# Kernel tuning notes

Hardware: AMD Instinct MI355X
Metric: run time of the kernel (lower is better)

Reference implementation:

```python
import jax, jax.numpy as jnp
import numpy as np

HEADS = 8
DIM_HEAD = 64
MAX_REL = 200  # max_rel_dist


def setup_inputs() -> dict:
    key = jax.random.key(0)
    ks = jax.random.split(key, 5)
    B, N, D = 4, 2048, 512
    x = jax.random.normal(ks[0], (B, N, D), dtype=jnp.float32)
    temporal_mask = jax.random.randint(ks[1], (N, N), 0, 2, dtype=jnp.int32)
    gamma = jnp.ones((D,), jnp.float32)
    beta = jnp.zeros((D,), jnp.float32)
    Wqkv = jax.random.normal(ks[2], (D, 3 * HEADS * DIM_HEAD), dtype=jnp.float32) * 0.02
    Wout = jax.random.normal(ks[3], (HEADS * DIM_HEAD, D), dtype=jnp.float32) * 0.02
    bout = jnp.zeros((D,), jnp.float32)
    rel_table = jax.random.normal(ks[4], (2 * MAX_REL - 1,), dtype=jnp.float32) * 0.02
    return {"x": x, "gamma": gamma, "beta": beta, "Wqkv": Wqkv, "Wout": Wout,
            "bout": bout, "rel_table": rel_table, "temporal_mask": temporal_mask}


def reference(x, gamma, beta, Wqkv, Wout, bout, rel_table, temporal_mask):
    B, N, D = x.shape
    scale = DIM_HEAD ** -0.5
    # LayerNorm
    mu = jnp.mean(x, axis=-1, keepdims=True)
    var = jnp.mean(jnp.square(x - mu), axis=-1, keepdims=True)
    xn = (x - mu) * jax.lax.rsqrt(var + 1e-5) * gamma + beta
    # QKV projection (no bias), split heads: b n (h d) -> b h n d
    qkv = xn @ Wqkv  # [B, N, 3*H*d]
    q, k, v = jnp.split(qkv, 3, axis=-1)
    split = lambda t: t.reshape(B, N, HEADS, DIM_HEAD).transpose(0, 2, 1, 3)
    q, k, v = split(q), split(k), split(v)
    # scores with learned relative-position bias
    dots = jnp.einsum('bhnd,bhmd->bhnm', q, k) * scale  # [B,H,N,N]
    idx = jnp.arange(N)
    rel = jnp.clip(idx[:, None] - idx[None, :], -(MAX_REL - 1), MAX_REL - 1) + MAX_REL - 1
    dots = dots + rel_table[rel][None, None, :, :]
    # temporal mask (0 -> -inf); large negative for grad safety
    dots = jnp.where(temporal_mask[None, None, :, :] == 0, jnp.float32(-1e9), dots)
    attn = jax.nn.softmax(dots, axis=-1)
    out = jnp.einsum('bhnm,bhmd->bhnd', attn, v)
    out = out.transpose(0, 2, 1, 3).reshape(B, N, HEADS * DIM_HEAD)
    return out @ Wout + bout
```

## Files before the change

### kernel.cpp

```cpp
#include <hip/hip_runtime.h>

typedef __attribute__((ext_vector_type(8))) short bf16x8;
typedef __attribute__((ext_vector_type(4))) short bf16x4;
typedef __attribute__((ext_vector_type(4))) float f32x4;
typedef unsigned short ushort_t;

#define B_ 4
#define H_ 8
#define N_ 2048
#define D_ 512
#define MAXREL 199

__device__ __forceinline__ ushort_t f2bf(float f) {
    union { float f; unsigned u; } v; v.f = f;
    unsigned r = v.u + 0x7fffu + ((v.u >> 16) & 1u);
    return (ushort_t)(r >> 16);
}
__device__ __forceinline__ ushort_t f2bf_fast(float f) {
    union { float f; unsigned u; } v; v.f = f;
    return (ushort_t)((v.u + 0x8000u) >> 16);
}
__device__ __forceinline__ float bf2f(ushort_t u) {
    union { unsigned u; float f; } v; v.u = ((unsigned)u) << 16;
    return v.f;
}
__device__ __forceinline__ void gl_lds16(const ushort_t* g, ushort_t* l) {
    __builtin_amdgcn_global_load_lds(
        (const __attribute__((address_space(1))) void*)g,
        (__attribute__((address_space(3))) void*)l,
        16, 0, 0);
}

__global__ __launch_bounds__(256) void ln_kernel(const float* __restrict__ x,
                                                 const float* __restrict__ gamma,
                                                 const float* __restrict__ beta,
                                                 ushort_t* __restrict__ xn) {
    __shared__ float sbuf[4];
    const int row = blockIdx.x;
    const int t = threadIdx.x;
    const float* xr = x + (size_t)row * D_;

    float v0 = xr[t];
    float v1 = xr[t + 256];

    float s = v0 + v1;
    for (int o = 32; o > 0; o >>= 1) s += __shfl_down(s, o);
    if ((t & 63) == 0) sbuf[t >> 6] = s;
    __syncthreads();
    float mu = (sbuf[0] + sbuf[1] + sbuf[2] + sbuf[3]) * (1.0f / D_);
    __syncthreads();

    float d0 = v0 - mu, d1 = v1 - mu;
    float s2 = d0 * d0 + d1 * d1;
    for (int o = 32; o > 0; o >>= 1) s2 += __shfl_down(s2, o);
    if ((t & 63) == 0) sbuf[t >> 6] = s2;
    __syncthreads();
    float var = (sbuf[0] + sbuf[1] + sbuf[2] + sbuf[3]) * (1.0f / D_);
    float rs = rsqrtf(var + 1e-5f);

    ushort_t* yr = xn + (size_t)row * D_;
    yr[t]       = f2bf(d0 * rs * gamma[t]       + beta[t]);
    yr[t + 256] = f2bf(d1 * rs * gamma[t + 256] + beta[t + 256]);
}

__global__ __launch_bounds__(256) void wtrans_kernel(const float* __restrict__ W,
                                                     ushort_t* __restrict__ Wt,
                                                     int K, int Nn) {
    __shared__ float tile[32][33];
    const int bx = blockIdx.x * 32;
    const int by = blockIdx.y * 32;
    const int tx = threadIdx.x & 31, ty = threadIdx.x >> 5;
    #pragma unroll
    for (int i = 0; i < 32; i += 8)
        tile[ty + i][tx] = W[(size_t)(by + ty + i) * Nn + bx + tx];
    __syncthreads();
    #pragma unroll
    for (int i = 0; i < 32; i += 8)
        Wt[(size_t)(bx + ty + i) * K + by + tx] = f2bf(tile[tx][ty + i]);
}

__global__ __launch_bounds__(256) void bias_pack_kernel(const float* __restrict__ rel,
                                                        const int* __restrict__ mask,
                                                        ushort_t* __restrict__ bp) {
    int idx = blockIdx.x * 256 + threadIdx.x;
    int n = idx >> 11, m = idx & 2047;
    int dl = n - m;
    dl = dl < -MAXREL ? -MAXREL : (dl > MAXREL ? MAXREL : dl);
    float v = (mask[idx] == 0) ? -1e9f : rel[dl + MAXREL];
    int jt = m >> 6, m16 = m & 15, nt = (m >> 4) & 3;
    bp[((size_t)n * 32 + jt) * 64 + m16 * 4 + nt] = f2bf(v);
}

__global__ __launch_bounds__(256) void gemm_qkv(const ushort_t* __restrict__ A,
                                                const ushort_t* __restrict__ Bt,
                                                ushort_t* __restrict__ qb,
                                                ushort_t* __restrict__ kb,
                                                ushort_t* __restrict__ vb) {
    __shared__ ushort_t As[128 * 32];
    __shared__ ushort_t Bs[128 * 32];
    const int t = threadIdx.x;
    const int lane = t & 63, w = t >> 6;
    const int m16 = lane & 15, quad = lane >> 4;
    const int wr = w >> 1, wc = w & 1;
    const int r0 = blockIdx.y * 128, c0 = blockIdx.x * 128;

    const ushort_t* Ag = A  + (size_t)(r0 + (t >> 2)) * D_ + (t & 3) * 8;
    const ushort_t* Bg = Bt + (size_t)(c0 + (t >> 2)) * D_ + (t & 3) * 8;
    ushort_t* AsW = As + w * 512;
    ushort_t* BsW = Bs + w * 512;

    f32x4 acc[4][4];
    #pragma unroll
    for (int i = 0; i < 4; i++)
        #pragma unroll
        for (int j = 0; j < 4; j++) acc[i][j] = (f32x4){0.f, 0.f, 0.f, 0.f};

    for (int k0 = 0; k0 < D_; k0 += 32) {
        gl_lds16(Ag + k0, AsW);
        gl_lds16(Ag + k0 + (size_t)64 * D_, AsW + 2048);
        gl_lds16(Bg + k0, BsW);
        gl_lds16(Bg + k0 + (size_t)64 * D_, BsW + 2048);
        __syncthreads();
        bf16x8 af[4], bfr[4];
        #pragma unroll
        for (int rt = 0; rt < 4; rt++)
            af[rt] = *(const bf16x8*)(As + (wr * 64 + rt * 16 + m16) * 32 + quad * 8);
        #pragma unroll
        for (int ct = 0; ct < 4; ct++)
            bfr[ct] = *(const bf16x8*)(Bs + (wc * 64 + ct * 16 + m16) * 32 + quad * 8);
        #pragma unroll
        for (int rt = 0; rt < 4; rt++)
            #pragma unroll
            for (int ct = 0; ct < 4; ct++)
                acc[rt][ct] = __builtin_amdgcn_mfma_f32_16x16x32_bf16(af[rt], bfr[ct], acc[rt][ct], 0, 0, 0);
        __syncthreads();
    }

    #pragma unroll
    for (int ct = 0; ct < 4; ct++) {
        int cc = c0 + wc * 64 + ct * 16;
        int which = cc >> 9;
        int h = (cc >> 6) & 7;
        int d = (cc & 63) + m16;
        #pragma unroll
        for (int rt = 0; rt < 4; rt++) {
            int rowb = r0 + wr * 64 + rt * 16 + quad * 4;
            int b = rowb >> 11, n0 = rowb & 2047;
            if (which == 0) {
                #pragma unroll
                for (int r = 0; r < 4; r++)
                    qb[((size_t)((b * H_ + h) * N_ + n0 + r)) * 64 + d] = f2bf(acc[rt][ct][r] * 0.125f);
            } else if (which == 1) {
                #pragma unroll
                for (int r = 0; r < 4; r++)
                    kb[((size_t)((b * H_ + h) * N_ + n0 + r)) * 64 + d] = f2bf(acc[rt][ct][r]);
            } else {
                union { ushort_t u4[4]; unsigned long long ll; } pk;
                #pragma unroll
                for (int r = 0; r < 4; r++) pk.u4[r] = f2bf(acc[rt][ct][r]);
                *(unsigned long long*)(vb + ((size_t)((b * H_ + h) * 64 + d)) * N_ + n0) = pk.ll;
            }
        }
    }
}

__global__ __launch_bounds__(256) void gemm_out(const ushort_t* __restrict__ A,
                                                const ushort_t* __restrict__ Bt,
                                                const float* __restrict__ bias,
                                                float* __restrict__ C) {
    __shared__ ushort_t As[64 * 32];
    __shared__ ushort_t Bs[128 * 32];
    const int t = threadIdx.x;
    const int lane = t & 63, w = t >> 6;
    const int m16 = lane & 15, quad = lane >> 4;
    const int wr = w >> 1, wc = w & 1;
    const int r0 = blockIdx.y * 64, c0 = blockIdx.x * 128;

    const ushort_t* Ag = A  + (size_t)(r0 + (t >> 2)) * D_ + (t & 3) * 8;
    const ushort_t* Bg = Bt + (size_t)(c0 + (t >> 2)) * D_ + (t & 3) * 8;
    ushort_t* AsW = As + w * 512;
    ushort_t* BsW = Bs + w * 512;

    f32x4 acc[2][4];
    #pragma unroll
    for (int i = 0; i < 2; i++)
        #pragma unroll
        for (int j = 0; j < 4; j++) acc[i][j] = (f32x4){0.f, 0.f, 0.f, 0.f};

    for (int k0 = 0; k0 < D_; k0 += 32) {
        gl_lds16(Ag + k0, AsW);
        gl_lds16(Bg + k0, BsW);
        gl_lds16(Bg + k0 + (size_t)64 * D_, BsW + 2048);
        __syncthreads();
        bf16x8 af[2], bfr[4];
        #pragma unroll
        for (int mf = 0; mf < 2; mf++)
            af[mf] = *(const bf16x8*)(As + (wr * 32 + mf * 16 + m16) * 32 + quad * 8);
        #pragma unroll
        for (int nt = 0; nt < 4; nt++)
            bfr[nt] = *(const bf16x8*)(Bs + (wc * 64 + nt * 16 + m16) * 32 + quad * 8);
        #pragma unroll
        for (int mf = 0; mf < 2; mf++)
            #pragma unroll
            for (int nt = 0; nt < 4; nt++)
                acc[mf][nt] = __builtin_amdgcn_mfma_f32_16x16x32_bf16(af[mf], bfr[nt], acc[mf][nt], 0, 0, 0);
        __syncthreads();
    }

    #pragma unroll
    for (int mf = 0; mf < 2; mf++) {
        #pragma unroll
        for (int nt = 0; nt < 4; nt++) {
            int col = c0 + wc * 64 + nt * 16 + m16;
            int row0 = r0 + wr * 32 + mf * 16 + quad * 4;
            float bv = bias[col];
            #pragma unroll
            for (int r = 0; r < 4; r++)
                C[(size_t)(row0 + r) * 512 + col] = acc[mf][nt][r] + bv;
        }
    }
}

__global__ __launch_bounds__(256, 3) void attn_mfma(const ushort_t* __restrict__ qb,
                                                    const ushort_t* __restrict__ kb,
                                                    const ushort_t* __restrict__ vb,
                                                    const ushort_t* __restrict__ bp,
                                                    ushort_t* __restrict__ attn) {
    __shared__ ushort_t Ks[2][64 * 64];
    __shared__ ushort_t Vs[2][64 * 64];
    __shared__ ushort_t p_s[4 * 2][16 * 64];

    const int t = threadIdx.x;
    const int w = t >> 6, lane = t & 63;
    const int m16 = lane & 15, quad = lane >> 4;
    const int id = blockIdx.x;
    const int bh = id & 31;
    const int qt = id >> 5;
    const int b = bh >> 3, h = bh & 7;
    const int n0w = qt * 128 + w * 32;

    const int srow0 = t >> 3, scb = t & 7;
    const int srow1 = srow0 + 32;
    const int soff0 = srow0 * 64 + (scb ^ (srow0 & 7)) * 8;
    const int soff1 = srow1 * 64 + (scb ^ (srow1 & 7)) * 8;
    const ushort_t* kgbase = kb + ((size_t)bh * N_) * 64;
    const ushort_t* vgbase = vb + ((size_t)bh * 64) * N_;

    const ushort_t* qpb = qb + ((size_t)(bh * N_ + n0w + m16)) * 64 + quad * 8;
    bf16x8 qa[2][2];
    qa[0][0] = *(const bf16x8*)(qpb);
    qa[0][1] = *(const bf16x8*)(qpb + 32);
    qa[1][0] = *(const bf16x8*)(qpb + 16 * 64);
    qa[1][1] = *(const bf16x8*)(qpb + 16 * 64 + 32);

    {
        bf16x8 k0 = *(const bf16x8*)(kgbase + (size_t)srow0 * 64 + scb * 8);
        bf16x8 k1 = *(const bf16x8*)(kgbase + (size_t)srow1 * 64 + scb * 8);
        bf16x8 v0 = *(const bf16x8*)(vgbase + (size_t)srow0 * N_ + scb * 8);
        bf16x8 v1 = *(const bf16x8*)(vgbase + (size_t)srow1 * N_ + scb * 8);
        *(bf16x8*)(&Ks[0][soff0]) = k0;
        *(bf16x8*)(&Ks[0][soff1]) = k1;
        *(bf16x8*)(&Vs[0][soff0]) = v0;
        *(bf16x8*)(&Vs[0][soff1]) = v1;
    }
    __syncthreads();

    f32x4 o[2][4];
    #pragma unroll
    for (int mf = 0; mf < 2; mf++)
        #pragma unroll
        for (int nt = 0; nt < 4; nt++) o[mf][nt] = (f32x4){0.f, 0.f, 0.f, 0.f};
    float rsum[2][4] = {};

    for (int jt = 0; jt < 32; jt++) {
        const int buf = jt & 1;
        const int j0 = jt * 64;
        const bool more = (jt < 31);

        bf16x8 kst0, kst1, vst0, vst1;
        if (more) {
            const ushort_t* kg = kgbase + (size_t)(j0 + 64) * 64;
            const ushort_t* vg = vgbase + (j0 + 64);
            kst0 = *(const bf16x8*)(kg + (size_t)srow0 * 64 + scb * 8);
            kst1 = *(const bf16x8*)(kg + (size_t)srow1 * 64 + scb * 8);
            vst0 = *(const bf16x8*)(vg + (size_t)srow0 * N_ + scb * 8);
            vst1 = *(const bf16x8*)(vg + (size_t)srow1 * N_ + scb * 8);
        }

        bf16x4 bcur[2][4];
        #pragma unroll
        for (int mf = 0; mf < 2; mf++)
            #pragma unroll
            for (int r = 0; r < 4; r++) {
                int n = n0w + mf * 16 + quad * 4 + r;
                bcur[mf][r] = *(const bf16x4*)(bp + ((size_t)n * 32 + jt) * 64 + m16 * 4);
            }

        f32x4 s[2][4];
        #pragma unroll
        for (int nt = 0; nt < 4; nt++) {
            int kr = nt * 16 + m16;
            bf16x8 kf0 = *(const bf16x8*)(&Ks[buf][kr * 64 + ((quad) ^ (kr & 7)) * 8]);
            bf16x8 kf1 = *(const bf16x8*)(&Ks[buf][kr * 64 + ((quad + 4) ^ (kr & 7)) * 8]);
            #pragma unroll
            for (int mf = 0; mf < 2; mf++) {
                f32x4 a2 = (f32x4){0.f, 0.f, 0.f, 0.f};
                a2 = __builtin_amdgcn_mfma_f32_16x16x32_bf16(qa[mf][0], kf0, a2, 0, 0, 0);
                a2 = __builtin_amdgcn_mfma_f32_16x16x32_bf16(qa[mf][1], kf1, a2, 0, 0, 0);
                s[mf][nt] = a2;
            }
        }

        #pragma unroll
        for (int mf = 0; mf < 2; mf++) {
            ushort_t* pw = p_s[w * 2 + mf];
            #pragma unroll
            for (int nt = 0; nt < 4; nt++) {
                int chunk = nt * 2 + (m16 >> 3), pos = m16 & 7;
                #pragma unroll
                for (int r = 0; r < 4; r++) {
                    float p = __expf(s[mf][nt][r] + bf2f((ushort_t)bcur[mf][r][nt]));
                    rsum[mf][r] += p;
                    int row = quad * 4 + r;
                    pw[row * 64 + ((chunk ^ (row & 7)) << 3) + pos] = f2bf_fast(p);
                }
            }
        }

        bf16x8 pa[2][2];
        #pragma unroll
        for (int mf = 0; mf < 2; mf++) {
            const ushort_t* pw = p_s[w * 2 + mf];
            pa[mf][0] = *(const bf16x8*)(pw + m16 * 64 + ((quad ^ (m16 & 7)) << 3));
            pa[mf][1] = *(const bf16x8*)(pw + m16 * 64 + (((quad + 4) ^ (m16 & 7)) << 3));
        }

        #pragma unroll
        for (int nt = 0; nt < 4; nt++) {
            int d = nt * 16 + m16;
            bf16x8 vf0 = *(const bf16x8*)(&Vs[buf][d * 64 + ((quad) ^ (d & 7)) * 8]);
            bf16x8 vf1 = *(const bf16x8*)(&Vs[buf][d * 64 + ((quad + 4) ^ (d & 7)) * 8]);
            #pragma unroll
            for (int mf = 0; mf < 2; mf++) {
                o[mf][nt] = __builtin_amdgcn_mfma_f32_16x16x32_bf16(pa[mf][0], vf0, o[mf][nt], 0, 0, 0);
                o[mf][nt] = __builtin_amdgcn_mfma_f32_16x16x32_bf16(pa[mf][1], vf1, o[mf][nt], 0, 0, 0);
            }
        }

        if (more) {
            *(bf16x8*)(&Ks[buf ^ 1][soff0]) = kst0;
            *(bf16x8*)(&Ks[buf ^ 1][soff1]) = kst1;
            *(bf16x8*)(&Vs[buf ^ 1][soff0]) = vst0;
            *(bf16x8*)(&Vs[buf ^ 1][soff1]) = vst1;
        }
        __syncthreads();
    }

    #pragma unroll
    for (int mf = 0; mf < 2; mf++)
        #pragma unroll
        for (int r = 0; r < 4; r++) {
            float t2 = rsum[mf][r];
            t2 += __shfl_xor(t2, 1);
            t2 += __shfl_xor(t2, 2);
            t2 += __shfl_xor(t2, 4);
            t2 += __shfl_xor(t2, 8);
            float inv = 1.0f / t2;
            int n = n0w + mf * 16 + quad * 4 + r;
            ushort_t* orow = attn + ((size_t)(b * N_ + n)) * 512 + h * 64 + m16;
            #pragma unroll
            for (int nt = 0; nt < 4; nt++) orow[nt * 16] = f2bf(o[mf][nt][r] * inv);
        }
}

extern "C" void kernel_launch(void* const* d_in, const int* in_sizes, int n_in,
                              void* d_out, int out_size, void* d_ws, size_t ws_size,
                              hipStream_t stream) {
    const float* x     = (const float*)d_in[0];
    const float* gamma = (const float*)d_in[1];
    const float* beta  = (const float*)d_in[2];
    const float* Wqkv  = (const float*)d_in[3];
    const float* Wout  = (const float*)d_in[4];
    const float* bout  = (const float*)d_in[5];
    const float* rel   = (const float*)d_in[6];
    const int*   mask  = (const int*)d_in[7];
    float* out = (float*)d_out;

    char* wsb = (char*)d_ws;
    ushort_t* xn    = (ushort_t*)(wsb);
    ushort_t* attnb = (ushort_t*)(wsb + ( 8u << 20));
    ushort_t* qb    = (ushort_t*)(wsb + (16u << 20));
    ushort_t* kb    = (ushort_t*)(wsb + (24u << 20));
    ushort_t* vb    = (ushort_t*)(wsb + (32u << 20));
    ushort_t* WqkvT = (ushort_t*)(wsb + (40u << 20));
    ushort_t* WoutT = (ushort_t*)(wsb + (42u << 20));
    ushort_t* bp    = (ushort_t*)(wsb + (44u << 20));

    wtrans_kernel<<<dim3(1536 / 32, 512 / 32), 256, 0, stream>>>(Wqkv, WqkvT, 512, 1536);
    wtrans_kernel<<<dim3(512 / 32, 512 / 32), 256, 0, stream>>>(Wout, WoutT, 512, 512);
    bias_pack_kernel<<<(N_ * N_) / 256, 256, 0, stream>>>(rel, mask, bp);

    ln_kernel<<<B_ * N_, 256, 0, stream>>>(x, gamma, beta, xn);

    gemm_qkv<<<dim3(1536 / 128, 8192 / 128), 256, 0, stream>>>(xn, WqkvT, qb, kb, vb);

    attn_mfma<<<512, 256, 0, stream>>>(qb, kb, vb, bp, attnb);

    gemm_out<<<dim3(512 / 128, 8192 / 64), 256, 0, stream>>>(attnb, WoutT, bout, out);
}
```

Before: 214.1 us.

## Merge prep kernels into one launch and use 8-wave attention blocks

Folds the weight transposes, bias packing and LayerNorm into a single prep kernel that dispatches on block index, which saves three launches. The attention kernel moves to 512 threads per block, each wave owning 16 query rows instead of 32, so each K/V tile staged in LDS is shared by twice as many waves and each thread loads half as much. The trade is that every wave now reads the K/V fragments from LDS for half as much MFMA work, which raises the LDS traffic per FLOP. The launch bound also changes to (512, 4), which may cap registers.

New measurement: 200.4 us. -6.4%, faster.

```diff
diff --git a/kernel.cpp b/kernel.cpp
--- a/kernel.cpp
+++ b/kernel.cpp
@@ -31,64 +31,73 @@
         16, 0, 0);
 }
 
-__global__ __launch_bounds__(256) void ln_kernel(const float* __restrict__ x,
-                                                 const float* __restrict__ gamma,
-                                                 const float* __restrict__ beta,
-                                                 ushort_t* __restrict__ xn) {
-    __shared__ float sbuf[4];
-    const int row = blockIdx.x;
+#define PREP_BIAS  16384
+#define PREP_LN    8192
+#define PREP_WQ    768
+#define PREP_WO    256
+__global__ __launch_bounds__(256) void prep_kernel(const float* __restrict__ x,
+                                                   const float* __restrict__ gamma,
+                                                   const float* __restrict__ beta,
+                                                   ushort_t* __restrict__ xn,
+                                                   const float* __restrict__ Wqkv,
+                                                   ushort_t* __restrict__ WqkvT,
+                                                   const float* __restrict__ Wout,
+                                                   ushort_t* __restrict__ WoutT,
+                                                   const float* __restrict__ rel,
+                                                   const int* __restrict__ mask,
+                                                   ushort_t* __restrict__ bp) {
+    __shared__ float smem[32 * 33];
+    const int blk = blockIdx.x;
     const int t = threadIdx.x;
-    const float* xr = x + (size_t)row * D_;
-
-    float v0 = xr[t];
-    float v1 = xr[t + 256];
-
-    float s = v0 + v1;
-    for (int o = 32; o > 0; o >>= 1) s += __shfl_down(s, o);
-    if ((t & 63) == 0) sbuf[t >> 6] = s;
-    __syncthreads();
-    float mu = (sbuf[0] + sbuf[1] + sbuf[2] + sbuf[3]) * (1.0f / D_);
-    __syncthreads();
-
-    float d0 = v0 - mu, d1 = v1 - mu;
-    float s2 = d0 * d0 + d1 * d1;
-    for (int o = 32; o > 0; o >>= 1) s2 += __shfl_down(s2, o);
-    if ((t & 63) == 0) sbuf[t >> 6] = s2;
-    __syncthreads();
-    float var = (sbuf[0] + sbuf[1] + sbuf[2] + sbuf[3]) * (1.0f / D_);
-    float rs = rsqrtf(var + 1e-5f);
-
-    ushort_t* yr = xn + (size_t)row * D_;
-    yr[t]       = f2bf(d0 * rs * gamma[t]       + beta[t]);
-    yr[t + 256] = f2bf(d1 * rs * gamma[t + 256] + beta[t + 256]);
-}
-
-__global__ __launch_bounds__(256) void wtrans_kernel(const float* __restrict__ W,
-                                                     ushort_t* __restrict__ Wt,
-                                                     int K, int Nn) {
-    __shared__ float tile[32][33];
-    const int bx = blockIdx.x * 32;
-    const int by = blockIdx.y * 32;
-    const int tx = threadIdx.x & 31, ty = threadIdx.x >> 5;
-    #pragma unroll
-    for (int i = 0; i < 32; i += 8)
-        tile[ty + i][tx] = W[(size_t)(by + ty + i) * Nn + bx + tx];
-    __syncthreads();
-    #pragma unroll
-    for (int i = 0; i < 32; i += 8)
-        Wt[(size_t)(bx + ty + i) * K + by + tx] = f2bf(tile[tx][ty + i]);
-}
-
-__global__ __launch_bounds__(256) void bias_pack_kernel(const float* __restrict__ rel,
-                                                        const int* __restrict__ mask,
-                                                        ushort_t* __restrict__ bp) {
-    int idx = blockIdx.x * 256 + threadIdx.x;
-    int n = idx >> 11, m = idx & 2047;
-    int dl = n - m;
-    dl = dl < -MAXREL ? -MAXREL : (dl > MAXREL ? MAXREL : dl);
-    float v = (mask[idx] == 0) ? -1e9f : rel[dl + MAXREL];
-    int jt = m >> 6, m16 = m & 15, nt = (m >> 4) & 3;
-    bp[((size_t)n * 32 + jt) * 64 + m16 * 4 + nt] = f2bf(v);
+
+    if (blk < PREP_BIAS) {
+        int idx = blk * 256 + t;
+        int n = idx >> 11, m = idx & 2047;
+        int dl = n - m;
+        dl = dl < -MAXREL ? -MAXREL : (dl > MAXREL ? MAXREL : dl);
+        float v = (mask[idx] == 0) ? -1e9f : rel[dl + MAXREL];
+        int jt = m >> 6, m16 = m & 15, nt = (m >> 4) & 3;
+        bp[((size_t)n * 32 + jt) * 64 + m16 * 4 + nt] = f2bf(v);
+    } else if (blk < PREP_BIAS + PREP_LN) {
+        const int row = blk - PREP_BIAS;
+        const float* xr = x + (size_t)row * D_;
+        float v0 = xr[t];
+        float v1 = xr[t + 256];
+        float s = v0 + v1;
+        for (int o = 32; o > 0; o >>= 1) s += __shfl_down(s, o);
+        if ((t & 63) == 0) smem[t >> 6] = s;
+        __syncthreads();
+        float mu = (smem[0] + smem[1] + smem[2] + smem[3]) * (1.0f / D_);
+        __syncthreads();
+        float d0 = v0 - mu, d1 = v1 - mu;
+        float s2 = d0 * d0 + d1 * d1;
+        for (int o = 32; o > 0; o >>= 1) s2 += __shfl_down(s2, o);
+        if ((t & 63) == 0) smem[t >> 6] = s2;
+        __syncthreads();
+        float var = (smem[0] + smem[1] + smem[2] + smem[3]) * (1.0f / D_);
+        float rs = rsqrtf(var + 1e-5f);
+        ushort_t* yr = xn + (size_t)row * D_;
+        yr[t]       = f2bf(d0 * rs * gamma[t]       + beta[t]);
+        yr[t + 256] = f2bf(d1 * rs * gamma[t + 256] + beta[t + 256]);
+    } else {
+        const float* W; ushort_t* Wt; int Nn, i;
+        if (blk < PREP_BIAS + PREP_LN + PREP_WQ) {
+            i = blk - (PREP_BIAS + PREP_LN); W = Wqkv; Wt = WqkvT; Nn = 1536;
+        } else {
+            i = blk - (PREP_BIAS + PREP_LN + PREP_WQ); W = Wout; Wt = WoutT; Nn = 512;
+        }
+        const int nb = Nn >> 5;
+        const int bx = (i % nb) * 32, by = (i / nb) * 32;
+        const int tx = t & 31, ty = t >> 5;
+        float (*tile)[33] = (float(*)[33])smem;
+        #pragma unroll
+        for (int k = 0; k < 32; k += 8)
+            tile[ty + k][tx] = W[(size_t)(by + ty + k) * Nn + bx + tx];
+        __syncthreads();
+        #pragma unroll
+        for (int k = 0; k < 32; k += 8)
+            Wt[(size_t)(bx + ty + k) * 512 + by + tx] = f2bf(tile[tx][ty + k]);
+    }
 }
 
 __global__ __launch_bounds__(256) void gemm_qkv(const ushort_t* __restrict__ A,
@@ -221,14 +230,14 @@
     }
 }
 
-__global__ __launch_bounds__(256, 3) void attn_mfma(const ushort_t* __restrict__ qb,
+__global__ __launch_bounds__(512, 4) void attn_mfma(const ushort_t* __restrict__ qb,
                                                     const ushort_t* __restrict__ kb,
                                                     const ushort_t* __restrict__ vb,
                                                     const ushort_t* __restrict__ bp,
                                                     ushort_t* __restrict__ attn) {
     __shared__ ushort_t Ks[2][64 * 64];
     __shared__ ushort_t Vs[2][64 * 64];
-    __shared__ ushort_t p_s[4 * 2][16 * 64];
+    __shared__ ushort_t p_s[8][16 * 64];
 
     const int t = threadIdx.x;
     const int w = t >> 6, lane = t & 63;
@@ -237,140 +246,101 @@
     const int bh = id & 31;
     const int qt = id >> 5;
     const int b = bh >> 3, h = bh & 7;
-    const int n0w = qt * 128 + w * 32;
-
-    const int srow0 = t >> 3, scb = t & 7;
-    const int srow1 = srow0 + 32;
-    const int soff0 = srow0 * 64 + (scb ^ (srow0 & 7)) * 8;
-    const int soff1 = srow1 * 64 + (scb ^ (srow1 & 7)) * 8;
+    const int n0w = qt * 128 + w * 16;
+
+    const int srow = t >> 3, scb = t & 7;
+    const int soff = srow * 64 + (scb ^ (srow & 7)) * 8;
     const ushort_t* kgbase = kb + ((size_t)bh * N_) * 64;
     const ushort_t* vgbase = vb + ((size_t)bh * 64) * N_;
 
     const ushort_t* qpb = qb + ((size_t)(bh * N_ + n0w + m16)) * 64 + quad * 8;
-    bf16x8 qa[2][2];
-    qa[0][0] = *(const bf16x8*)(qpb);
-    qa[0][1] = *(const bf16x8*)(qpb + 32);
-    qa[1][0] = *(const bf16x8*)(qpb + 16 * 64);
-    qa[1][1] = *(const bf16x8*)(qpb + 16 * 64 + 32);
-
-    {
-        bf16x8 k0 = *(const bf16x8*)(kgbase + (size_t)srow0 * 64 + scb * 8);
-        bf16x8 k1 = *(const bf16x8*)(kgbase + (size_t)srow1 * 64 + scb * 8);
-        bf16x8 v0 = *(const bf16x8*)(vgbase + (size_t)srow0 * N_ + scb * 8);
-        bf16x8 v1 = *(const bf16x8*)(vgbase + (size_t)srow1 * N_ + scb * 8);
-        *(bf16x8*)(&Ks[0][soff0]) = k0;
-        *(bf16x8*)(&Ks[0][soff1]) = k1;
-        *(bf16x8*)(&Vs[0][soff0]) = v0;
-        *(bf16x8*)(&Vs[0][soff1]) = v1;
-    }
+    bf16x8 qa0 = *(const bf16x8*)(qpb);
+    bf16x8 qa1 = *(const bf16x8*)(qpb + 32);
+
+    *(bf16x8*)(&Ks[0][soff]) = *(const bf16x8*)(kgbase + (size_t)srow * 64 + scb * 8);
+    *(bf16x8*)(&Vs[0][soff]) = *(const bf16x8*)(vgbase + (size_t)srow * N_ + scb * 8);
     __syncthreads();
 
-    f32x4 o[2][4];
-    #pragma unroll
-    for (int mf = 0; mf < 2; mf++)
-        #pragma unroll
-        for (int nt = 0; nt < 4; nt++) o[mf][nt] = (f32x4){0.f, 0.f, 0.f, 0.f};
-    float rsum[2][4] = {};
+    f32x4 o[4];
+    #pragma unroll
+    for (int nt = 0; nt < 4; nt++) o[nt] = (f32x4){0.f, 0.f, 0.f, 0.f};
+    float rsum[4] = {};
 
     for (int jt = 0; jt < 32; jt++) {
         const int buf = jt & 1;
         const int j0 = jt * 64;
         const bool more = (jt < 31);
 
-        bf16x8 kst0, kst1, vst0, vst1;
+        bf16x8 kst, vst;
         if (more) {
-            const ushort_t* kg = kgbase + (size_t)(j0 + 64) * 64;
-            const ushort_t* vg = vgbase + (j0 + 64);
-            kst0 = *(const bf16x8*)(kg + (size_t)srow0 * 64 + scb * 8);
-            kst1 = *(const bf16x8*)(kg + (size_t)srow1 * 64 + scb * 8);
-            vst0 = *(const bf16x8*)(vg + (size_t)srow0 * N_ + scb * 8);
-            vst1 = *(const bf16x8*)(vg + (size_t)srow1 * N_ + scb * 8);
-        }
-
-        bf16x4 bcur[2][4];
-        #pragma unroll
-        for (int mf = 0; mf < 2; mf++)
-            #pragma unroll
-            for (int r = 0; r < 4; r++) {
-                int n = n0w + mf * 16 + quad * 4 + r;
-                bcur[mf][r] = *(const bf16x4*)(bp + ((size_t)n * 32 + jt) * 64 + m16 * 4);
-            }
-
-        f32x4 s[2][4];
+            kst = *(const bf16x8*)(kgbase + (size_t)(j0 + 64 + srow) * 64 + scb * 8);
+            vst = *(const bf16x8*)(vgbase + (size_t)srow * N_ + j0 + 64 + scb * 8);
+        }
+
+        bf16x4 bcur[4];
+        #pragma unroll
+        for (int r = 0; r < 4; r++) {
+            int n = n0w + quad * 4 + r;
+            bcur[r] = *(const bf16x4*)(bp + ((size_t)n * 32 + jt) * 64 + m16 * 4);
+        }
+
+        f32x4 s[4];
         #pragma unroll
         for (int nt = 0; nt < 4; nt++) {
             int kr = nt * 16 + m16;
             bf16x8 kf0 = *(const bf16x8*)(&Ks[buf][kr * 64 + ((quad) ^ (kr & 7)) * 8]);
             bf16x8 kf1 = *(const bf16x8*)(&Ks[buf][kr * 64 + ((quad + 4) ^ (kr & 7)) * 8]);
+            f32x4 a2 = (f32x4){0.f, 0.f, 0.f, 0.f};
+            a2 = __builtin_amdgcn_mfma_f32_16x16x32_bf16(qa0, kf0, a2, 0, 0, 0);
+            a2 = __builtin_amdgcn_mfma_f32_16x16x32_bf16(qa1, kf1, a2, 0, 0, 0);
+            s[nt] = a2;
+        }
+
+        ushort_t* pw = p_s[w];
+        #pragma unroll
+        for (int nt = 0; nt < 4; nt++) {
+            int chunk = nt * 2 + (m16 >> 3), pos = m16 & 7;
             #pragma unroll
-            for (int mf = 0; mf < 2; mf++) {
-                f32x4 a2 = (f32x4){0.f, 0.f, 0.f, 0.f};
-                a2 = __builtin_amdgcn_mfma_f32_16x16x32_bf16(qa[mf][0], kf0, a2, 0, 0, 0);
-                a2 = __builtin_amdgcn_mfma_f32_16x16x32_bf16(qa[mf][1], kf1, a2, 0, 0, 0);
-                s[mf][nt] = a2;
+            for (int r = 0; r < 4; r++) {
+                float p = __expf(s[nt][r] + bf2f((ushort_t)bcur[r][nt]));
+                rsum[r] += p;
+                int row = quad * 4 + r;
+                pw[row * 64 + ((chunk ^ (row & 7)) << 3) + pos] = f2bf_fast(p);
             }
         }
 
-        #pragma unroll
-        for (int mf = 0; mf < 2; mf++) {
-            ushort_t* pw = p_s[w * 2 + mf];
-            #pragma unroll
-            for (int nt = 0; nt < 4; nt++) {
-                int chunk = nt * 2 + (m16 >> 3), pos = m16 & 7;
-                #pragma unroll
-                for (int r = 0; r < 4; r++) {
-                    float p = __expf(s[mf][nt][r] + bf2f((ushort_t)bcur[mf][r][nt]));
-                    rsum[mf][r] += p;
-                    int row = quad * 4 + r;
-                    pw[row * 64 + ((chunk ^ (row & 7)) << 3) + pos] = f2bf_fast(p);
-                }
-            }
-        }
-
-        bf16x8 pa[2][2];
-        #pragma unroll
-        for (int mf = 0; mf < 2; mf++) {
-            const ushort_t* pw = p_s[w * 2 + mf];
-            pa[mf][0] = *(const bf16x8*)(pw + m16 * 64 + ((quad ^ (m16 & 7)) << 3));
-            pa[mf][1] = *(const bf16x8*)(pw + m16 * 64 + (((quad + 4) ^ (m16 & 7)) << 3));
-        }
+        bf16x8 pa0 = *(const bf16x8*)(pw + m16 * 64 + ((quad ^ (m16 & 7)) << 3));
+        bf16x8 pa1 = *(const bf16x8*)(pw + m16 * 64 + (((quad + 4) ^ (m16 & 7)) << 3));
 
         #pragma unroll
         for (int nt = 0; nt < 4; nt++) {
             int d = nt * 16 + m16;
             bf16x8 vf0 = *(const bf16x8*)(&Vs[buf][d * 64 + ((quad) ^ (d & 7)) * 8]);
             bf16x8 vf1 = *(const bf16x8*)(&Vs[buf][d * 64 + ((quad + 4) ^ (d & 7)) * 8]);
-            #pragma unroll
-            for (int mf = 0; mf < 2; mf++) {
-                o[mf][nt] = __builtin_amdgcn_mfma_f32_16x16x32_bf16(pa[mf][0], vf0, o[mf][nt], 0, 0, 0);
-                o[mf][nt] = __builtin_amdgcn_mfma_f32_16x16x32_bf16(pa[mf][1], vf1, o[mf][nt], 0, 0, 0);
-            }
+            o[nt] = __builtin_amdgcn_mfma_f32_16x16x32_bf16(pa0, vf0, o[nt], 0, 0, 0);
+            o[nt] = __builtin_amdgcn_mfma_f32_16x16x32_bf16(pa1, vf1, o[nt], 0, 0, 0);
         }
 
         if (more) {
-            *(bf16x8*)(&Ks[buf ^ 1][soff0]) = kst0;
-            *(bf16x8*)(&Ks[buf ^ 1][soff1]) = kst1;
-            *(bf16x8*)(&Vs[buf ^ 1][soff0]) = vst0;
-            *(bf16x8*)(&Vs[buf ^ 1][soff1]) = vst1;
-        }
-        __syncthreads();
-    }
-
-    #pragma unroll
-    for (int mf = 0; mf < 2; mf++)
-        #pragma unroll
-        for (int r = 0; r < 4; r++) {
-            float t2 = rsum[mf][r];
-            t2 += __shfl_xor(t2, 1);
-            t2 += __shfl_xor(t2, 2);
-            t2 += __shfl_xor(t2, 4);
-            t2 += __shfl_xor(t2, 8);
-            float inv = 1.0f / t2;
-            int n = n0w + mf * 16 + quad * 4 + r;
-            ushort_t* orow = attn + ((size_t)(b * N_ + n)) * 512 + h * 64 + m16;
-            #pragma unroll
-            for (int nt = 0; nt < 4; nt++) orow[nt * 16] = f2bf(o[mf][nt][r] * inv);
-        }
+            *(bf16x8*)(&Ks[buf ^ 1][soff]) = kst;
+            *(bf16x8*)(&Vs[buf ^ 1][soff]) = vst;
+        }
+        __syncthreads();
+    }
+
+    #pragma unroll
+    for (int r = 0; r < 4; r++) {
+        float t2 = rsum[r];
+        t2 += __shfl_xor(t2, 1);
+        t2 += __shfl_xor(t2, 2);
+        t2 += __shfl_xor(t2, 4);
+        t2 += __shfl_xor(t2, 8);
+        float inv = 1.0f / t2;
+        int n = n0w + quad * 4 + r;
+        ushort_t* orow = attn + ((size_t)(b * N_ + n)) * 512 + h * 64 + m16;
+        #pragma unroll
+        for (int nt = 0; nt < 4; nt++) orow[nt * 16] = f2bf(o[nt][r] * inv);
+    }
 }
 
 extern "C" void kernel_launch(void* const* d_in, const int* in_sizes, int n_in,
@@ -396,15 +366,12 @@
     ushort_t* WoutT = (ushort_t*)(wsb + (42u << 20));
     ushort_t* bp    = (ushort_t*)(wsb + (44u << 20));
 
-    wtrans_kernel<<<dim3(1536 / 32, 512 / 32), 256, 0, stream>>>(Wqkv, WqkvT, 512, 1536);
-    wtrans_kernel<<<dim3(512 / 32, 512 / 32), 256, 0, stream>>>(Wout, WoutT, 512, 512);
-    bias_pack_kernel<<<(N_ * N_) / 256, 256, 0, stream>>>(rel, mask, bp);
-
-    ln_kernel<<<B_ * N_, 256, 0, stream>>>(x, gamma, beta, xn);
+    prep_kernel<<<PREP_BIAS + PREP_LN + PREP_WQ + PREP_WO, 256, 0, stream>>>(
+        x, gamma, beta, xn, Wqkv, WqkvT, Wout, WoutT, rel, mask, bp);
 
     gemm_qkv<<<dim3(1536 / 128, 8192 / 128), 256, 0, stream>>>(xn, WqkvT, qb, kb, vb);
 
-    attn_mfma<<<512, 256, 0, stream>>>(qb, kb, vb, bp, attnb);
+    attn_mfma<<<512, 512, 0, stream>>>(qb, kb, vb, bp, attnb);
 
     gemm_out<<<dim3(512 / 128, 8192 / 64), 256, 0, stream>>>(attnb, WoutT, bout, out);
 }
```
